# Kernel tuning notes

Measured on AMD Instinct MI355X. Metric: run time of the kernel, lower is better.

## Reference

```python
import jax, jax.numpy as jnp
import numpy as np

N_NODES = 50000
N_EDGES = 800000
D = 64
N_LAYERS = 5
N_GRAPHS = 256
N_CLASSES = 10
BN_EPS = 1e-5


def setup_inputs() -> dict:
    key = jax.random.key(0)
    ks = jax.random.split(key, 16)
    s = 1.0 / np.sqrt(D)
    return {
        "X": jax.random.normal(ks[0], (N_NODES, D), jnp.float32),
        "edge_index": jax.random.randint(ks[1], (2, N_EDGES), 0, N_NODES, jnp.int64),
        "batch": jnp.sort(jax.random.randint(ks[2], (N_NODES,), 0, N_GRAPHS, jnp.int64)),
        "Wk": jax.random.normal(ks[3], (N_LAYERS, D, D), jnp.float32) * s,
        "Wq": jax.random.normal(ks[4], (N_LAYERS, D, D), jnp.float32) * s,
        "Wv": jax.random.normal(ks[5], (N_LAYERS, D, D), jnp.float32) * s,
        "Ws": jax.random.normal(ks[6], (N_LAYERS, D, D), jnp.float32) * s,
        "bk": jnp.zeros((N_LAYERS, D), jnp.float32),
        "bq": jnp.zeros((N_LAYERS, D), jnp.float32),
        "bv": jnp.zeros((N_LAYERS, D), jnp.float32),
        "bconv": jnp.zeros((N_LAYERS, D), jnp.float32),
        "gamma": jnp.ones((N_LAYERS, D), jnp.float32),
        "beta": jnp.zeros((N_LAYERS, D), jnp.float32),
        "Wlin": jax.random.normal(ks[7], (D, N_CLASSES), jnp.float32) * s,
        "blin": jnp.zeros((N_CLASSES,), jnp.float32),
    }


def _res_gated_conv(x, src, dst, Wk, Wq, Wv, Ws, bk, bq, bv, b):
    # PyG ResGatedGraphConv: out_i = W_skip x_i + b + sum_{j->i} sigmoid(K x_i + Q x_j) * (V x_j)
    k = x @ Wk + bk  # [N, D]
    q = x @ Wq + bq
    v = x @ Wv + bv
    eta = jax.nn.sigmoid(k[dst] + q[src])         # [E, D] gate
    agg = jax.ops.segment_sum(eta * v[src], dst, num_segments=x.shape[0])
    return agg + x @ Ws + b


def _batch_norm(x, gamma, beta):
    mean = jnp.mean(x, axis=0)
    var = jnp.mean(jnp.square(x - mean), axis=0)  # biased, as torch BN training
    return (x - mean) * jax.lax.rsqrt(var + BN_EPS) * gamma + beta


def reference(X, edge_index, batch, Wk, Wq, Wv, Ws, bk, bq, bv, bconv, gamma, beta, Wlin, blin):
    src, dst = edge_index[0], edge_index[1]
    h = X
    for l in range(N_LAYERS):  # dropout_prob = 0 -> dropout is identity
        h = _res_gated_conv(h, src, dst, Wk[l], Wq[l], Wv[l], Ws[l], bk[l], bq[l], bv[l], bconv[l])
        h = jax.nn.relu(h)
        h = _batch_norm(h, gamma[l], beta[l])
    # global mean pool over graphs
    sums = jax.ops.segment_sum(h, batch, num_segments=N_GRAPHS)
    counts = jax.ops.segment_sum(jnp.ones((h.shape[0], 1), h.dtype), batch, num_segments=N_GRAPHS)
    pooled = sums / jnp.maximum(counts, 1.0)
    logits = pooled @ Wlin + blin
    return jax.nn.softmax(logits, axis=-1)
```

## Files before the change

kernel.cpp:

```cpp
#include <hip/hip_runtime.h>

#define NN 50000
#define NE 800000
#define DD 64
#define NL 5
#define NG 256
#define NC 10
#define BN_EPS 1e-5f
#define NCHUNK ((NN + 255) / 256)
#define GROWS 128
#define GT (GROWS / 16)
#define SAW 68
#define GEMM_BLOCKS ((NN + GROWS - 1) / GROWS)
#define NNS (NN + 8)
#define PADDEG(d) (((d) + 7) & ~7)
#define DEG_BLOCKS ((NE + 255) / 256)
#define WPREP_BLOCKS ((NL * 2048 + 255) / 256)
#define FILL_BLOCKS DEG_BLOCKS
#define PAD_BLOCKS NCHUNK

typedef __attribute__((ext_vector_type(8))) short bf16x8;
typedef __attribute__((ext_vector_type(4))) float f32x4;

__device__ inline float bf2f(unsigned short u) {
    return __uint_as_float((unsigned)u << 16);
}
__device__ inline unsigned short f2bf(float x) {
    unsigned u = __float_as_uint(x);
    u += 0x7FFFu + ((u >> 16) & 1u);
    return (unsigned short)(u >> 16);
}

__device__ inline unsigned int pack_bf16x2(float a, float b) {
    unsigned int ua = __float_as_uint(a);
    unsigned int ub = __float_as_uint(b);
    ua += 0x7FFFu + ((ua >> 16) & 1u);
    ub += 0x7FFFu + ((ub >> 16) & 1u);
    return (ub & 0xFFFF0000u) | (ua >> 16);
}

__device__ inline void split_bf16(float x, short& h, short& l) {
    const unsigned u  = __float_as_uint(x);
    const unsigned hb = u & 0xFFFF0000u;
    h = (short)(hb >> 16);
    const float lo = x - __uint_as_float(hb);
    l = (short)(__float_as_uint(lo) >> 16);
}

__device__ inline float p_eq(unsigned p) { return __uint_as_float(p << 16); }
__device__ inline float p_v(unsigned p)  { return __uint_as_float(p & 0xFFFF0000u); }

#define GPAIR(ek, pa, pb, acc) { \
    const float t1_ = fmaf(ek, p_eq(pa), 1.f); \
    const float t2_ = fmaf(ek, p_eq(pb), 1.f); \
    const float R_  = __builtin_amdgcn_rcpf(t1_ * t2_); \
    acc = fmaf(fmaf(p_v(pb), t1_, p_v(pa) * t2_), R_, acc); }

#define GCOLS(ekx, eky, p, accx, accy) { \
    const float t1_ = fmaf(ekx, p_eq(p.x), 1.f); \
    const float t2_ = fmaf(eky, p_eq(p.y), 1.f); \
    const float R_  = __builtin_amdgcn_rcpf(t1_ * t2_); \
    accx = fmaf(p_v(p.x), R_ * t2_, accx); \
    accy = fmaf(p_v(p.y), R_ * t1_, accy); }

template<int F32>
__device__ __forceinline__ void gemm_body(
    const void* __restrict__ HinV,
    const bf16x8* __restrict__ whbuf, const bf16x8* __restrict__ wlbuf,
    const float* __restrict__ bk, const float* __restrict__ bq,
    const float* __restrict__ bv, const float* __restrict__ bs,
    const float* __restrict__ prevStats,
    const float* __restrict__ prevGamma, const float* __restrict__ prevBeta,
    unsigned short* __restrict__ Kq, unsigned int* __restrict__ QVq,
    unsigned short* __restrict__ Hq, const int gb)
{
    __shared__ unsigned int sA[GROWS * SAW];
    __shared__ float sAB[128];
    const int tid = threadIdx.x;

    if (!F32) {
        if (tid < 64) {
            const float invN = 1.0f / (float)NN;
            const float mean = prevStats[tid] * invN;
            const float var  = prevStats[64 + tid] * invN - mean * mean;
            const float inv  = rsqrtf(var + BN_EPS);
            const float a = inv * prevGamma[tid];
            sAB[tid]      = a;
            sAB[64 + tid] = prevBeta[tid] - mean * a;
        }
        __syncthreads();
    }

    const int row0 = gb * GROWS;
    if (F32) {
        const float* X = (const float*)HinV;
        for (int i = tid; i < GROWS * 16; i += 256) {
            const int row = i >> 4;
            const int k4  = (i & 15) * 4;
            float4 x = make_float4(0.f, 0.f, 0.f, 0.f);
            if (row0 + row < NN)
                x = *(const float4*)(X + (size_t)(row0 + row) * DD + k4);
            const float xs[4] = {x.x, x.y, x.z, x.w};
            unsigned int* dst = &sA[row * SAW + k4];
#pragma unroll
            for (int j = 0; j < 4; j++) {
                short hs, ls;
                split_bf16(xs[j], hs, ls);
                dst[j] = ((unsigned int)(unsigned short)hs << 16) | (unsigned short)ls;
            }
        }
    } else {
        const unsigned short* Hin = (const unsigned short*)HinV;
        for (int i = tid; i < GROWS * 8; i += 256) {
            const int row = i >> 3;
            const int cb  = (i & 7) * 8;
            const int q   = cb >> 4;
            const int o16 = cb & 15;
            uint4 v = make_uint4(0u, 0u, 0u, 0u);
            if (row0 + row < NN)
                v = *(const uint4*)&Hin[((size_t)q * NN + row0 + row) * 16 + o16];
            const unsigned ws[4] = {v.x, v.y, v.z, v.w};
            unsigned int* dst = &sA[row * SAW + cb];
#pragma unroll
            for (int j = 0; j < 4; j++) {
                const float x0 = bf2f((unsigned short)(ws[j] & 0xFFFFu));
                const float x1 = bf2f((unsigned short)(ws[j] >> 16));
                const int c0 = cb + 2 * j, c1 = cb + 2 * j + 1;
                short hs, ls;
                split_bf16(fmaf(x0, sAB[c0], sAB[64 + c0]), hs, ls);
                dst[2 * j] = ((unsigned int)(unsigned short)hs << 16) | (unsigned short)ls;
                split_bf16(fmaf(x1, sAB[c1], sAB[64 + c1]), hs, ls);
                dst[2 * j + 1] = ((unsigned int)(unsigned short)hs << 16) | (unsigned short)ls;
            }
        }
    }

    const int wave = tid >> 6;
    const int lane = tid & 63;
    const int n15  = lane & 15;
    const int g    = lane >> 4;
    const int col  = wave * 16 + n15;

    bf16x8 wh[4][2], wl[4][2];
    {
        const int base = wave * 64 + lane;
#pragma unroll
        for (int m = 0; m < 4; m++)
#pragma unroll
            for (int c = 0; c < 2; c++) {
                const int idx = m * 512 + c * 256 + base;
                wh[m][c] = whbuf[idx];
                wl[m][c] = wlbuf[idx];
            }
    }

    const float bkc = bk[col], bqc = bq[col], bvc = bv[col], bsc = bs[col];
    __syncthreads();

#pragma unroll 1
    for (int t = 0; t < GT; t++) {
        const int rowbase = row0 + t * 16;
        if (rowbase >= NN) break;

        bf16x8 ah[2], al[2];
#pragma unroll
        for (int c = 0; c < 2; c++) {
            const uint4 u0 = *(const uint4*)&sA[(t * 16 + n15) * SAW + g * 8 + 32 * c];
            const uint4 u1 = *(const uint4*)&sA[(t * 16 + n15) * SAW + g * 8 + 32 * c + 4];
            const unsigned int us[8] = {u0.x, u0.y, u0.z, u0.w, u1.x, u1.y, u1.z, u1.w};
            bf16x8 h, l;
#pragma unroll
            for (int j = 0; j < 8; j++) {
                h[j] = (short)(us[j] >> 16);
                l[j] = (short)(us[j] & 0xFFFFu);
            }
            ah[c] = h; al[c] = l;
        }

        f32x4 acc[4];
#pragma unroll
        for (int m = 0; m < 4; m++) acc[m] = (f32x4){0.f, 0.f, 0.f, 0.f};

#pragma unroll
        for (int c = 0; c < 2; c++) {
#pragma unroll
            for (int m = 0; m < 4; m++) {
                acc[m] = __builtin_amdgcn_mfma_f32_16x16x32_bf16(ah[c], wh[m][c], acc[m], 0, 0, 0);
                acc[m] = __builtin_amdgcn_mfma_f32_16x16x32_bf16(al[c], wh[m][c], acc[m], 0, 0, 0);
                acc[m] = __builtin_amdgcn_mfma_f32_16x16x32_bf16(ah[c], wl[m][c], acc[m], 0, 0, 0);
            }
        }

#pragma unroll
        for (int r = 0; r < 4; r++) {
            const int row = rowbase + g * 4 + r;
            const size_t o  = ((size_t)wave * NN  + row) * 16 + n15;
            const size_t oq = ((size_t)wave * NNS + row) * 16 + n15;
            Kq[o]   = f2bf(__expf(-(acc[0][r] + bkc)));
            QVq[oq] = pack_bf16x2(__expf(-(acc[1][r] + bqc)), acc[2][r] + bvc);
            Hq[o]   = f2bf(acc[3][r] + bsc);
        }
    }
}

__global__ __launch_bounds__(256) void prep_kernel(
    const int* __restrict__ ei, int* __restrict__ deg,
    const float* __restrict__ Wk, const float* __restrict__ Wq,
    const float* __restrict__ Wv, const float* __restrict__ Ws,
    bf16x8* __restrict__ whbuf, bf16x8* __restrict__ wlbuf,
    unsigned int* __restrict__ QVq)
{
    const int bid = blockIdx.x;
    if (bid < DEG_BLOCKS) {
        const int e = bid * 256 + threadIdx.x;
        if (e < NE) atomicAdd(&deg[ei[NE + e]], 1);
        return;
    }
    if (bid == DEG_BLOCKS && threadIdx.x < 64) {
        const int q = threadIdx.x >> 4, c = threadIdx.x & 15;
        QVq[((size_t)q * NNS + NN) * 16 + c] = 0u;
    }
    const int t = (bid - DEG_BLOCKS) * 256 + threadIdx.x;
    if (t >= NL * 2048) return;
    const int lane = t & 63;
    const int w    = (t >> 6) & 3;
    const int c    = (t >> 8) & 1;
    const int m    = (t >> 9) & 3;
    const int l    = t >> 11;

    const float* Wm4[4] = {Wk, Wq, Wv, Ws};
    const float* W = Wm4[m] + l * 4096;
    const int col = w * 16 + (lane & 15);
    const int g   = lane >> 4;

    bf16x8 h, lo;
#pragma unroll
    for (int j = 0; j < 8; j++) {
        const int k = g * 8 + j + 32 * c;
        short hs, ls;
        split_bf16(W[k * DD + col], hs, ls);
        h[j] = hs; lo[j] = ls;
    }
    whbuf[t] = h;
    wlbuf[t] = lo;
}

__global__ __launch_bounds__(256) void scan_partial_kernel(
    const int* __restrict__ deg, int* __restrict__ psums)
{
    __shared__ int ls[256];
    const int i = blockIdx.x * 256 + threadIdx.x;
    ls[threadIdx.x] = (i < NN) ? PADDEG(deg[i]) : 0;
    __syncthreads();
    for (int off = 128; off > 0; off >>= 1) {
        if (threadIdx.x < off) ls[threadIdx.x] += ls[threadIdx.x + off];
        __syncthreads();
    }
    if (threadIdx.x == 0) psums[blockIdx.x] = ls[0];
}

__global__ void scan_offsets_kernel(int* __restrict__ psums, int* __restrict__ rowst)
{
    if (threadIdx.x == 0) {
        int running = 0;
        for (int i = 0; i < NCHUNK; i++) {
            int t = psums[i];
            psums[i] = running;
            running += t;
        }
        rowst[NN] = running;
    }
}

__global__ __launch_bounds__(256) void scan_final_kernel(
    const int* __restrict__ deg, const int* __restrict__ psums,
    int* __restrict__ rowst, int* __restrict__ cursor)
{
    __shared__ int ls[256];
    const int i = blockIdx.x * 256 + threadIdx.x;
    const int x = (i < NN) ? PADDEG(deg[i]) : 0;
    ls[threadIdx.x] = x;
    __syncthreads();
    for (int off = 1; off < 256; off <<= 1) {
        int v = (threadIdx.x >= off) ? ls[threadIdx.x - off] : 0;
        __syncthreads();
        ls[threadIdx.x] += v;
        __syncthreads();
    }
    if (i < NN) {
        const int excl = psums[blockIdx.x] + ls[threadIdx.x] - x;
        rowst[i]  = excl;
        cursor[i] = excl;
    }
}

__global__ __launch_bounds__(256) void gfp_kernel(
    const float* __restrict__ X,
    const bf16x8* __restrict__ whbuf, const bf16x8* __restrict__ wlbuf,
    const float* __restrict__ bk, const float* __restrict__ bq,
    const float* __restrict__ bv, const float* __restrict__ bs,
    unsigned short* __restrict__ Kq, unsigned int* __restrict__ QVq,
    unsigned short* __restrict__ Hq,
    const int* __restrict__ ei, int* __restrict__ cursor,
    const int* __restrict__ rowst, const int* __restrict__ deg,
    unsigned short* __restrict__ csr16)
{
    const int bid = blockIdx.x;
    if (bid < GEMM_BLOCKS) {
        gemm_body<1>(X, whbuf, wlbuf, bk, bq, bv, bs,
                     nullptr, nullptr, nullptr, Kq, QVq, Hq, bid);
        return;
    }
    if (bid < GEMM_BLOCKS + FILL_BLOCKS) {
        const int e = (bid - GEMM_BLOCKS) * 256 + threadIdx.x;
        if (e < NE) {
            const int src = ei[e];
            const int dst = ei[NE + e];
            csr16[atomicAdd(&cursor[dst], 1)] = (unsigned short)src;
        }
        return;
    }
    const int n = (bid - GEMM_BLOCKS - FILL_BLOCKS) * 256 + threadIdx.x;
    if (n >= NN) return;
    const int end = rowst[n + 1];
    for (int i = rowst[n] + deg[n]; i < end; i++) csr16[i] = (unsigned short)NN;
}

__global__ __launch_bounds__(256) void gemm4_mfma(
    const void* __restrict__ HinV,
    const bf16x8* __restrict__ whbuf, const bf16x8* __restrict__ wlbuf,
    const float* __restrict__ bk, const float* __restrict__ bq,
    const float* __restrict__ bv, const float* __restrict__ bs,
    const float* __restrict__ prevStats,
    const float* __restrict__ prevGamma, const float* __restrict__ prevBeta,
    unsigned short* __restrict__ Kq, unsigned int* __restrict__ QVq,
    unsigned short* __restrict__ Hq)
{
    gemm_body<0>(HinV, whbuf, wlbuf, bk, bq, bv, bs,
                 prevStats, prevGamma, prevBeta, Kq, QVq, Hq, blockIdx.x);
}

#define GATHER_BLOCKS (8 * 782)
__global__ __launch_bounds__(256) void gather_kernel(
    const int* __restrict__ rowst, const unsigned short* __restrict__ csr16,
    const unsigned short* __restrict__ Kq, const unsigned int* __restrict__ QVq,
    unsigned short* Hq, float* __restrict__ stats)
{
    const int tid  = threadIdx.x;
    const int wv   = tid >> 6;
    const int lane = tid & 63;
    const int eoff = lane >> 3;
    const int cp   = lane & 7;

    const int j       = blockIdx.x;
    const int xcd     = j & 7;
    const int quarter = xcd >> 1;
    const int half    = xcd & 1;
    const int nodebase = ((j >> 3) * 2 + half) * 32 + wv * 8;

    const unsigned* Kq32 = (const unsigned*)(Kq + (size_t)quarter * NN * 16);
    const uint2*    Qq2  = (const uint2*)(QVq + (size_t)quarter * NNS * 16);
    unsigned*       Hq32 = (unsigned*)(Hq + (size_t)quarter * NN * 16);

    float se = 0.f, s2e = 0.f, so = 0.f, s2o = 0.f;

    for (int t = 0; t < 4; t++) {
        const int n0 = nodebase + 2 * t;
        if (n0 >= NN) break;
        const int n1 = n0 + 1;
        const unsigned ho0 = (unsigned)(n0 * 8 + cp);
        const unsigned ho1 = (unsigned)(n1 * 8 + cp);
        unsigned h0p = 0u, h1p = 0u;
        if (eoff == 0) {
            h0p = Hq32[ho0];
            h1p = Hq32[ho1];
        }
        const unsigned k0p = Kq32[ho0];
        const unsigned k1p = Kq32[ho1];
        const float ek00 = bf2f((unsigned short)(k0p & 0xFFFFu));
        const float ek01 = bf2f((unsigned short)(k0p >> 16));
        const float ek10 = bf2f((unsigned short)(k1p & 0xFFFFu));
        const float ek11 = bf2f((unsigned short)(k1p >> 16));
        const int e00 = rowst[n0], e01 = rowst[n1], e11 = rowst[n1 + 1];
        int nd0 = (e01 - e00) >> 3;
        int nd1 = (e11 - e01) >> 3;
        int ndm = min(nd0, nd1);
        nd0 -= ndm; nd1 -= ndm;
        int b0 = e00, b1 = e01;
        float a00 = 0.f, a01 = 0.f, a10 = 0.f, a11 = 0.f;

        while (ndm >= 2) {
            const unsigned s0 = *(const unsigned*)(csr16 + b0 + 2 * eoff);
            const unsigned s1 = *(const unsigned*)(csr16 + b1 + 2 * eoff);
            const uint2 p0a = Qq2[(s0 & 0xFFFFu) * 8u + cp];
            const uint2 p0b = Qq2[(s0 >> 16) * 8u + cp];
            const uint2 p1a = Qq2[(s1 & 0xFFFFu) * 8u + cp];
            const uint2 p1b = Qq2[(s1 >> 16) * 8u + cp];
            GPAIR(ek00, p0a.x, p0b.x, a00);
            GPAIR(ek01, p0a.y, p0b.y, a01);
            GPAIR(ek10, p1a.x, p1b.x, a10);
            GPAIR(ek11, p1a.y, p1b.y, a11);
            b0 += 16; b1 += 16; ndm -= 2;
        }
        if (ndm) {
            const int s0 = csr16[b0 + eoff];
            const int s1 = csr16[b1 + eoff];
            const uint2 p0 = Qq2[(unsigned)(s0 * 8 + cp)];
            const uint2 p1 = Qq2[(unsigned)(s1 * 8 + cp)];
            GCOLS(ek00, ek01, p0, a00, a01);
            GCOLS(ek10, ek11, p1, a10, a11);
            b0 += 8; b1 += 8;
        }
        while (nd0 >= 2) {
            const unsigned s0 = *(const unsigned*)(csr16 + b0 + 2 * eoff);
            const uint2 p0a = Qq2[(s0 & 0xFFFFu) * 8u + cp];
            const uint2 p0b = Qq2[(s0 >> 16) * 8u + cp];
            GPAIR(ek00, p0a.x, p0b.x, a00);
            GPAIR(ek01, p0a.y, p0b.y, a01);
            b0 += 16; nd0 -= 2;
        }
        if (nd0) {
            const int s0 = csr16[b0 + eoff];
            const uint2 p0 = Qq2[(unsigned)(s0 * 8 + cp)];
            GCOLS(ek00, ek01, p0, a00, a01);
        }
        while (nd1 >= 2) {
            const unsigned s1 = *(const unsigned*)(csr16 + b1 + 2 * eoff);
            const uint2 p1a = Qq2[(s1 & 0xFFFFu) * 8u + cp];
            const uint2 p1b = Qq2[(s1 >> 16) * 8u + cp];
            GPAIR(ek10, p1a.x, p1b.x, a10);
            GPAIR(ek11, p1a.y, p1b.y, a11);
            b1 += 16; nd1 -= 2;
        }
        if (nd1) {
            const int s1 = csr16[b1 + eoff];
            const uint2 p1 = Qq2[(unsigned)(s1 * 8 + cp)];
            GCOLS(ek10, ek11, p1, a10, a11);
        }

        a00 += __shfl_xor(a00, 8);  a00 += __shfl_xor(a00, 16); a00 += __shfl_xor(a00, 32);
        a01 += __shfl_xor(a01, 8);  a01 += __shfl_xor(a01, 16); a01 += __shfl_xor(a01, 32);
        a10 += __shfl_xor(a10, 8);  a10 += __shfl_xor(a10, 16); a10 += __shfl_xor(a10, 32);
        a11 += __shfl_xor(a11, 8);  a11 += __shfl_xor(a11, 16); a11 += __shfl_xor(a11, 32);

        if (eoff == 0) {
            const float o00 = fmaxf(bf2f((unsigned short)(h0p & 0xFFFFu)) + a00, 0.f);
            const float o01 = fmaxf(bf2f((unsigned short)(h0p >> 16))     + a01, 0.f);
            const float o10 = fmaxf(bf2f((unsigned short)(h1p & 0xFFFFu)) + a10, 0.f);
            const float o11 = fmaxf(bf2f((unsigned short)(h1p >> 16))     + a11, 0.f);
            const unsigned short b00 = f2bf(o00), b01 = f2bf(o01);
            const unsigned short b10 = f2bf(o10), b11 = f2bf(o11);
            Hq32[ho0] = ((unsigned)b01 << 16) | b00;
            Hq32[ho1] = ((unsigned)b11 << 16) | b10;
            const float r00 = bf2f(b00), r01 = bf2f(b01);
            const float r10 = bf2f(b10), r11 = bf2f(b11);
            se  += r00 + r10;  s2e += r00 * r00 + r10 * r10;
            so  += r01 + r11;  s2o += r01 * r01 + r11 * r11;
        }
    }

    __shared__ float ls[64], ls2[64];
    if (eoff == 0) {
        ls[wv * 16 + 2 * cp]      = se;  ls2[wv * 16 + 2 * cp]      = s2e;
        ls[wv * 16 + 2 * cp + 1]  = so;  ls2[wv * 16 + 2 * cp + 1]  = s2o;
    }
    __syncthreads();
    if (tid < 16) {
        const float a = ls[tid] + ls[16 + tid] + ls[32 + tid] + ls[48 + tid];
        const float b = ls2[tid] + ls2[16 + tid] + ls2[32 + tid] + ls2[48 + tid];
        atomicAdd(&stats[quarter * 16 + tid], a);
        atomicAdd(&stats[64 + quarter * 16 + tid], b);
    }
}

#define POOL_ROWS 64
__global__ __launch_bounds__(256) void pool_kernel(
    const unsigned short* __restrict__ Hq, const int* __restrict__ batch,
    float* __restrict__ psum, float* __restrict__ pcnt)
{
    const int sub = threadIdx.x >> 6;
    const int c  = threadIdx.x & 63;
    const int q  = c >> 4;
    const int cl = c & 15;
    const int r0 = (blockIdx.x * 4 + sub) * POOL_ROWS;
    if (r0 >= NN) return;
    const int r1 = min(r0 + POOL_ROWS, NN);
    const unsigned short* Hqq = Hq + (size_t)q * NN * 16;

    int cur = batch[r0];
    float acc = 0.f, cnt = 0.f;
    for (int r = r0; r < r1; r++) {
        const int g = batch[r];
        if (g != cur) {
            atomicAdd(&psum[cur * DD + c], acc);
            if (c == 0) atomicAdd(&pcnt[cur], cnt);
            acc = 0.f; cnt = 0.f; cur = g;
        }
        acc += bf2f(Hqq[(size_t)r * 16 + cl]);
        cnt += 1.f;
    }
    atomicAdd(&psum[cur * DD + c], acc);
    if (c == 0) atomicAdd(&pcnt[cur], cnt);
}

__global__ __launch_bounds__(256) void final_kernel(
    const float* __restrict__ psum, const float* __restrict__ pcnt,
    const float* __restrict__ stats,
    const float* __restrict__ gamma, const float* __restrict__ beta,
    const float* __restrict__ Wlin, const float* __restrict__ blin,
    float* __restrict__ out)
{
    const int g = blockIdx.x * blockDim.x + threadIdx.x;
    if (g >= NG) return;

    const float invc = 1.0f / fmaxf(pcnt[g], 1.0f);
    const float invN = 1.0f / (float)NN;
    float p[DD];
#pragma unroll
    for (int d = 0; d < DD; d++) {
        const float mean = stats[d] * invN;
        const float var  = stats[64 + d] * invN - mean * mean;
        const float inv  = rsqrtf(var + BN_EPS);
        const float a = inv * gamma[d];
        const float b = beta[d] - mean * a;
        p[d] = fmaf(psum[g * DD + d] * invc, a, b);
    }

    float logits[NC];
    float m = -1e30f;
#pragma unroll
    for (int c = 0; c < NC; c++) {
        float acc = blin[c];
#pragma unroll
        for (int d = 0; d < DD; d++) acc = fmaf(p[d], Wlin[d * NC + c], acc);
        logits[c] = acc;
        m = fmaxf(m, acc);
    }
    float sum = 0.f;
#pragma unroll
    for (int c = 0; c < NC; c++) {
        logits[c] = __expf(logits[c] - m);
        sum += logits[c];
    }
    const float inv = 1.f / sum;
#pragma unroll
    for (int c = 0; c < NC; c++) out[g * NC + c] = logits[c] * inv;
}

extern "C" void kernel_launch(void* const* d_in, const int* in_sizes, int n_in,
                              void* d_out, int out_size, void* d_ws, size_t ws_size,
                              hipStream_t stream)
{
    const float* X     = (const float*)d_in[0];
    const int*   ei    = (const int*)d_in[1];
    const int*   batch = (const int*)d_in[2];
    const float* Wk    = (const float*)d_in[3];
    const float* Wq    = (const float*)d_in[4];
    const float* Wv    = (const float*)d_in[5];
    const float* Ws    = (const float*)d_in[6];
    const float* bk    = (const float*)d_in[7];
    const float* bq    = (const float*)d_in[8];
    const float* bv    = (const float*)d_in[9];
    const float* bconv = (const float*)d_in[10];
    const float* gamma = (const float*)d_in[11];
    const float* beta  = (const float*)d_in[12];
    const float* Wlin  = (const float*)d_in[13];
    const float* blin  = (const float*)d_in[14];
    float* out = (float*)d_out;

    const size_t M  = (size_t)NN * DD;
    const size_t MQ = (size_t)4 * NNS * 16;
    unsigned short* Kq  = (unsigned short*)d_ws;
    unsigned int*   QVq = (unsigned int*)(Kq + M);
    unsigned short* H0q = (unsigned short*)(QVq + MQ);
    unsigned short* H1q = H0q + M;
    int*   deg   = (int*)(H1q + M);
    float* psum  = (float*)(deg + NN);
    float* pcnt  = psum + (size_t)NG * DD;
    float* stats = pcnt + NG;
    int* rowst  = (int*)(stats + NL * 128);
    int* cursor = rowst + NN + 1;
    int* psums  = cursor + NN;
    unsigned short* csr16 = (unsigned short*)(psums + 256);
    bf16x8* whbuf = (bf16x8*)(csr16 + NE + 8 * NN);
    bf16x8* wlbuf = whbuf + NL * 2048;

    const size_t zero_bytes = (size_t)(NN + NG * DD + NG + NL * 128) * sizeof(float);
    hipMemsetAsync(deg, 0, zero_bytes, stream);

    prep_kernel<<<DEG_BLOCKS + WPREP_BLOCKS, 256, 0, stream>>>(
        ei, deg, Wk, Wq, Wv, Ws, whbuf, wlbuf, QVq);

    scan_partial_kernel<<<NCHUNK, 256, 0, stream>>>(deg, psums);
    scan_offsets_kernel<<<1, 64, 0, stream>>>(psums, rowst);
    scan_final_kernel<<<NCHUNK, 256, 0, stream>>>(deg, psums, rowst, cursor);

    gfp_kernel<<<GEMM_BLOCKS + FILL_BLOCKS + PAD_BLOCKS, 256, 0, stream>>>(
        X, whbuf, wlbuf, bk, bq, bv, bconv,
        Kq, QVq, H0q, ei, cursor, rowst, deg, csr16);

    gather_kernel<<<GATHER_BLOCKS, 256, 0, stream>>>(
        rowst, csr16, Kq, QVq, H0q, stats);
    const void* hin = (const void*)H0q;
    for (int l = 1; l < NL; l++) {
        unsigned short* hout = (l & 1) ? H1q : H0q;
        gemm4_mfma<<<GEMM_BLOCKS, 256, 0, stream>>>(
            hin, whbuf + l * 2048, wlbuf + l * 2048,
            bk + l * 64, bq + l * 64, bv + l * 64, bconv + l * 64,
            stats + (l - 1) * 128, gamma + (l - 1) * 64, beta + (l - 1) * 64,
            Kq, QVq, hout);
        gather_kernel<<<GATHER_BLOCKS, 256, 0, stream>>>(
            rowst, csr16, Kq, QVq, hout, stats + l * 128);
        hin = (const void*)hout;
    }

    pool_kernel<<<(NN + 4 * POOL_ROWS - 1) / (4 * POOL_ROWS), 256, 0, stream>>>(
        (const unsigned short*)hin, batch, psum, pcnt);
    final_kernel<<<1, 256, 0, stream>>>(
        psum, pcnt, stats + 4 * 128, gamma + 4 * 64, beta + 4 * 64, Wlin, blin, out);
}
```

Baseline: 538.0 us.

## Partition CSR fill by XCD range, use exp2 in gemm, vectorize pool loads

The CSR fill pass now launches eight blocks per edge chunk. Each block handles only destinations in one eighth of the node range, chosen by block index modulo 8, so the atomics and scattered writes stay within one XCD's L2 slice. The price is reading the dst array eight times. The GEMM epilogue computes exp(-x) as a single fused multiply-add feeding the hardware exp2. The gather kernel carries the row-start value across iterations so it does one fewer load each time, and the pool kernel reads two bf16 values per 32-bit load with twice as many rows per block.

```diff
diff --git a/kernel.cpp b/kernel.cpp
--- a/kernel.cpp
+++ b/kernel.cpp
@@ -16,8 +16,12 @@
 #define PADDEG(d) (((d) + 7) & ~7)
 #define DEG_BLOCKS ((NE + 255) / 256)
 #define WPREP_BLOCKS ((NL * 2048 + 255) / 256)
-#define FILL_BLOCKS DEG_BLOCKS
+#define FCHK 2048
+#define FCHUNKS ((NE + FCHK - 1) / FCHK)
+#define FILLP_BLOCKS (8 * FCHUNKS)
+#define NRANGE (NN / 8)
 #define PAD_BLOCKS NCHUNK
+#define L2E 1.4426950408889634f
 
 typedef __attribute__((ext_vector_type(8))) short bf16x8;
 typedef __attribute__((ext_vector_type(4))) float f32x4;
@@ -154,7 +158,9 @@
             }
     }
 
-    const float bkc = bk[col], bqc = bq[col], bvc = bv[col], bsc = bs[col];
+    const float nbk = -bk[col] * L2E;
+    const float nbq = -bq[col] * L2E;
+    const float bvc = bv[col], bsc = bs[col];
     __syncthreads();
 
 #pragma unroll 1
@@ -196,8 +202,9 @@
             const int row = rowbase + g * 4 + r;
             const size_t o  = ((size_t)wave * NN  + row) * 16 + n15;
             const size_t oq = ((size_t)wave * NNS + row) * 16 + n15;
-            Kq[o]   = f2bf(__expf(-(acc[0][r] + bkc)));
-            QVq[oq] = pack_bf16x2(__expf(-(acc[1][r] + bqc)), acc[2][r] + bvc);
+            Kq[o]   = f2bf(__builtin_amdgcn_exp2f(fmaf(acc[0][r], -L2E, nbk)));
+            QVq[oq] = pack_bf16x2(__builtin_amdgcn_exp2f(fmaf(acc[1][r], -L2E, nbq)),
+                                  acc[2][r] + bvc);
             Hq[o]   = f2bf(acc[3][r] + bsc);
         }
     }
@@ -311,16 +318,24 @@
                      nullptr, nullptr, nullptr, Kq, QVq, Hq, bid);
         return;
     }
-    if (bid < GEMM_BLOCKS + FILL_BLOCKS) {
-        const int e = (bid - GEMM_BLOCKS) * 256 + threadIdx.x;
-        if (e < NE) {
-            const int src = ei[e];
+    if (bid < GEMM_BLOCKS + FILLP_BLOCKS) {
+        const int fid = bid - GEMM_BLOCKS;
+        const int r   = bid & 7;
+        const int o   = fid >> 3;
+        const int lo  = r * NRANGE;
+        const int hi  = lo + NRANGE;
+        const int e0  = o * FCHK;
+        const int e1  = min(e0 + FCHK, NE);
+        for (int e = e0 + threadIdx.x; e < e1; e += 256) {
             const int dst = ei[NE + e];
-            csr16[atomicAdd(&cursor[dst], 1)] = (unsigned short)src;
+            if (dst >= lo && dst < hi) {
+                const int src = ei[e];
+                csr16[atomicAdd(&cursor[dst], 1)] = (unsigned short)src;
+            }
         }
         return;
     }
-    const int n = (bid - GEMM_BLOCKS - FILL_BLOCKS) * 256 + threadIdx.x;
+    const int n = (bid - GEMM_BLOCKS - FILLP_BLOCKS) * 256 + threadIdx.x;
     if (n >= NN) return;
     const int end = rowst[n + 1];
     for (int i = rowst[n] + deg[n]; i < end; i++) csr16[i] = (unsigned short)NN;
@@ -363,6 +378,8 @@
     unsigned*       Hq32 = (unsigned*)(Hq + (size_t)quarter * NN * 16);
 
     float se = 0.f, s2e = 0.f, so = 0.f, s2o = 0.f;
+
+    int e00 = rowst[min(nodebase, NN)];
 
     for (int t = 0; t < 4; t++) {
         const int n0 = nodebase + 2 * t;
@@ -381,12 +398,13 @@
         const float ek01 = bf2f((unsigned short)(k0p >> 16));
         const float ek10 = bf2f((unsigned short)(k1p & 0xFFFFu));
         const float ek11 = bf2f((unsigned short)(k1p >> 16));
-        const int e00 = rowst[n0], e01 = rowst[n1], e11 = rowst[n1 + 1];
+        const int e01 = rowst[n1], e11 = rowst[n1 + 1];
         int nd0 = (e01 - e00) >> 3;
         int nd1 = (e11 - e01) >> 3;
         int ndm = min(nd0, nd1);
         nd0 -= ndm; nd1 -= ndm;
         int b0 = e00, b1 = e01;
+        e00 = e11;
         float a00 = 0.f, a01 = 0.f, a10 = 0.f, a11 = 0.f;
 
         while (ndm >= 2) {
@@ -478,28 +496,33 @@
     const unsigned short* __restrict__ Hq, const int* __restrict__ batch,
     float* __restrict__ psum, float* __restrict__ pcnt)
 {
-    const int sub = threadIdx.x >> 6;
-    const int c  = threadIdx.x & 63;
-    const int q  = c >> 4;
-    const int cl = c & 15;
-    const int r0 = (blockIdx.x * 4 + sub) * POOL_ROWS;
+    const int sub = threadIdx.x >> 5;
+    const int c   = threadIdx.x & 31;
+    const int q   = c >> 3;
+    const int p   = c & 7;
+    const int r0 = (blockIdx.x * 8 + sub) * POOL_ROWS;
     if (r0 >= NN) return;
     const int r1 = min(r0 + POOL_ROWS, NN);
-    const unsigned short* Hqq = Hq + (size_t)q * NN * 16;
+    const unsigned* Hqq = (const unsigned*)(Hq + (size_t)q * NN * 16);
+    const int col0 = q * 16 + 2 * p;
 
     int cur = batch[r0];
-    float acc = 0.f, cnt = 0.f;
+    float acc0 = 0.f, acc1 = 0.f, cnt = 0.f;
     for (int r = r0; r < r1; r++) {
         const int g = batch[r];
         if (g != cur) {
-            atomicAdd(&psum[cur * DD + c], acc);
+            atomicAdd(&psum[cur * DD + col0], acc0);
+            atomicAdd(&psum[cur * DD + col0 + 1], acc1);
             if (c == 0) atomicAdd(&pcnt[cur], cnt);
-            acc = 0.f; cnt = 0.f; cur = g;
-        }
-        acc += bf2f(Hqq[(size_t)r * 16 + cl]);
+            acc0 = 0.f; acc1 = 0.f; cnt = 0.f; cur = g;
+        }
+        const unsigned hv = Hqq[(size_t)r * 8 + p];
+        acc0 += bf2f((unsigned short)(hv & 0xFFFFu));
+        acc1 += bf2f((unsigned short)(hv >> 16));
         cnt += 1.f;
     }
-    atomicAdd(&psum[cur * DD + c], acc);
+    atomicAdd(&psum[cur * DD + col0], acc0);
+    atomicAdd(&psum[cur * DD + col0 + 1], acc1);
     if (c == 0) atomicAdd(&pcnt[cur], cnt);
 }
 
@@ -595,7 +618,7 @@
     scan_offsets_kernel<<<1, 64, 0, stream>>>(psums, rowst);
     scan_final_kernel<<<NCHUNK, 256, 0, stream>>>(deg, psums, rowst, cursor);
 
-    gfp_kernel<<<GEMM_BLOCKS + FILL_BLOCKS + PAD_BLOCKS, 256, 0, stream>>>(
+    gfp_kernel<<<GEMM_BLOCKS + FILLP_BLOCKS + PAD_BLOCKS, 256, 0, stream>>>(
         X, whbuf, wlbuf, bk, bq, bv, bconv,
         Kq, QVq, H0q, ei, cursor, rowst, deg, csr16);
 
@@ -614,7 +637,7 @@
         hin = (const void*)hout;
     }
 
-    pool_kernel<<<(NN + 4 * POOL_ROWS - 1) / (4 * POOL_ROWS), 256, 0, stream>>>(
+    pool_kernel<<<(NN + 8 * POOL_ROWS - 1) / (8 * POOL_ROWS), 256, 0, stream>>>(
         (const unsigned short*)hin, batch, psum, pcnt);
     final_kernel<<<1, 256, 0, stream>>>(
         psum, pcnt, stats + 4 * 128, gamma + 4 * 64, beta + 4 * 64, Wlin, blin, out);
```

Result: no change. 529.1 us (-1.7%).
